# Optimization experiments

Hardware: AMD Instinct MI355X
Metric: run time of the kernel (lower is better)

The kernel has to match this reference:

```python
import jax, jax.numpy as jnp
import numpy as np
import itertools

BINS_NUM = 35
BINS_SIZE = 9
ORDERS = (2, 3, 4, 5)

def _comb_idx(n, k):
    # combinations with replacement of indices 0..n-1, shape [ncomb, k]
    return np.array(list(itertools.combinations_with_replacement(range(n), k)), dtype=np.int32)

_COMB = {k: _comb_idx(BINS_SIZE, k) for k in ORDERS}


def setup_inputs() -> dict:
    key = jax.random.key(0)
    x = jax.random.normal(key, (1024, BINS_NUM * BINS_SIZE), dtype=jnp.float32)
    return {"x": x}


def reference(x) -> jnp.ndarray:
    B = x.shape[0]
    bins = x.reshape(B, BINS_NUM, BINS_SIZE)          # [B, 35, 9]
    parts = [bins]                                     # 'origin' slice first
    for k in ORDERS:
        idx = jnp.asarray(_COMB[k])                    # [ncomb_k, k]
        gathered = bins[:, :, idx]                     # [B, 35, ncomb_k, k]
        parts.append(jnp.prod(gathered, axis=-1))      # [B, 35, ncomb_k]
    # per-bin concat [origin, de2, de3, de4, de5], then flatten bins -> matches
    # torch's outer concat over bins since bin is the leading concat axis here.
    out = jnp.concatenate(parts, axis=-1)              # [B, 35, 2001]
    return out.reshape(B, -1)                          # [B, 70035]
```

## Files before the change

kernel.cpp:

```cpp
#include <hip/hip_runtime.h>

#define BSZ 9
#define NPB 2001
#define N2 45
#define N3 165
#define N4 495
#define O2 9
#define O3 54
#define O4 219
#define ONE_SLOT 714
#define LSZ 720
#define NBLOCKS 2048
#define STRIDE_T (NBLOCKS * 4)

#define WAVE_SYNC() asm volatile("s_waitcnt lgkmcnt(0)" ::: "memory")

constexpr unsigned pslot2(unsigned i, unsigned j) {
    return O2 + i * 9u - i * (i - 1u) / 2u + (j - i);
}

struct Tabs { unsigned short p2[N2]; unsigned short p3[N3]; unsigned short p4[N4]; };
constexpr Tabs make_tabs() {
    Tabs t{};
    { int p = 0;
      for (unsigned i = 0; i < 9; ++i)
          for (unsigned j = i; j < 9; ++j)
              t.p2[p++] = (unsigned short)(i | (j << 8)); }
    { int p = 0;
      for (unsigned a = 0; a < 9; ++a)
          for (unsigned b = a; b < 9; ++b) {
              const unsigned ps = pslot2(a, b);
              for (unsigned c = b; c < 9; ++c)
                  t.p3[p++] = (unsigned short)(ps | (c << 8));
          } }
    { int p = 0; unsigned ts = O3;
      for (unsigned a = 0; a < 9; ++a)
          for (unsigned b = a; b < 9; ++b)
              for (unsigned c = b; c < 9; ++c) {
                  for (unsigned d = c; d < 9; ++d)
                      t.p4[p++] = (unsigned short)(ts | (d << 8));
                  ++ts;
              } }
    return t;
}
__constant__ Tabs g_tabs = make_tabs();

struct Full { unsigned t[NPB]; };
constexpr Full make_full() {
    Full f{};
    for (unsigned j = 0; j < ONE_SLOT; ++j)
        f.t[j] = (4u * j) | ((4u * ONE_SLOT) << 16);
    { int p = ONE_SLOT; unsigned qs = O4;
      for (unsigned a = 0; a < 9; ++a)
          for (unsigned b = a; b < 9; ++b)
              for (unsigned c = b; c < 9; ++c)
                  for (unsigned d = c; d < 9; ++d) {
                      for (unsigned e = d; e < 9; ++e)
                          f.t[p++] = (4u * qs) | ((4u * e) << 16);
                      ++qs;
                  } }
    return f;
}
__constant__ Full g_full = make_full();

__global__ __launch_bounds__(256) void poly_expand_kernel(
        const float* __restrict__ x, float* __restrict__ out, int ntask) {
    __shared__ float L[4][LSZ];
    const int wave = threadIdx.x >> 6;
    const int lane = threadIdx.x & 63;
    const int w0 = blockIdx.x * 4 + wave;
    if (w0 >= ntask) return;
    float* const Lw = L[wave];

    const unsigned o     = (unsigned)w0 & 3u;
    const unsigned a     = (4u - o) & 3u;
    const unsigned mA    = (ONE_SLOT - a) >> 2;
    const unsigned mB0   = (ONE_SLOT - a + 3u) >> 2;
    const unsigned Mfull = (NPB - a) >> 2;
    float* const Ls = Lw + o;
    const char* const Lc = (const char*)Ls;
    const float4* const Af4 = (const float4*)(Lw + o + a);

    const unsigned t2 = (lane < N2) ? (unsigned)g_tabs.p2[lane] : 0u;
    unsigned t3[3], t4[8];
    #pragma unroll
    for (int k = 0; k < 3; ++k) { const int s = lane + 64 * k;
        t3[k] = (s < N3) ? (unsigned)g_tabs.p3[s] : 0u; }
    #pragma unroll
    for (int k = 0; k < 8; ++k) { const int s = lane + 64 * k;
        t4[k] = (s < N4) ? (unsigned)g_tabs.p4[s] : 0u; }

    const unsigned jb0 = a + 4u * mB0;
    unsigned bpk[6][4];
    #pragma unroll
    for (int k = 0; k < 6; ++k) {
        const unsigned idx = (unsigned)lane + 64u * k;
        #pragma unroll
        for (int e = 0; e < 4; ++e)
            bpk[k][e] = (idx < 321u) ? g_full.t[jb0 + 4u * idx + (unsigned)e] : 0u;
    }

    const unsigned z1s = a + 4u * mA, z1n = 4u * (mB0 - mA);
    const unsigned z2s = a + 4u * Mfull, z2n = (unsigned)NPB - z2s;
    int jm = -1;
    if ((unsigned)lane < a)                 jm = lane;
    else if ((unsigned)lane < a + z1n)      jm = (int)(z1s + ((unsigned)lane - a));
    else if ((unsigned)lane < a + z1n + z2n) jm = (int)(z2s + ((unsigned)lane - a - z1n));
    const unsigned mpk = (jm >= 0) ? g_full.t[jm] : 0u;

    for (int task = w0; task < ntask; task += STRIDE_T) {
        const unsigned rb = (unsigned)task * (unsigned)NPB;
        WAVE_SYNC();

        if (lane < 9)       Ls[lane] = x[(size_t)task * BSZ + lane];
        else if (lane == 9) Ls[ONE_SLOT] = 1.0f;
        WAVE_SYNC();
        if (lane < N2) Ls[O2 + lane] = Ls[t2 & 255u] * Ls[t2 >> 8];
        WAVE_SYNC();
        #pragma unroll
        for (int k = 0; k < 3; ++k) { const int s = lane + 64 * k;
            if (s < N3) Ls[O3 + s] = Ls[t3[k] & 255u] * Ls[t3[k] >> 8]; }
        WAVE_SYNC();
        #pragma unroll
        for (int k = 0; k < 8; ++k) { const int s = lane + 64 * k;
            if (s < N4) Ls[O4 + s] = Ls[t4[k] & 255u] * Ls[t4[k] >> 8]; }
        WAVE_SYNC();

        float4* const po4 = (float4*)(out + rb + a);

        #pragma unroll
        for (int k = 0; k < 3; ++k) {
            const unsigned m = (unsigned)lane + 64u * k;
            if (m < mA) po4[m] = Af4[m];
        }
        #pragma unroll
        for (int k = 0; k < 6; ++k) {
            const unsigned idx = (unsigned)lane + 64u * k;
            if (idx < 321u) {
                float r[4];
                #pragma unroll
                for (int e = 0; e < 4; ++e) {
                    const unsigned pk = bpk[k][e];
                    r[e] = *(const float*)(Lc + (pk & 0xFFFFu)) *
                           *(const float*)(Lc + (pk >> 16));
                }
                po4[mB0 + idx] = make_float4(r[0], r[1], r[2], r[3]);
            }
        }
        if (jm >= 0)
            out[rb + (unsigned)jm] = *(const float*)(Lc + (mpk & 0xFFFFu)) *
                                     *(const float*)(Lc + (mpk >> 16));
    }
}

extern "C" void kernel_launch(void* const* d_in, const int* in_sizes, int n_in,
                              void* d_out, int out_size, void* d_ws, size_t ws_size,
                              hipStream_t stream) {
    const float* x = (const float*)d_in[0];
    float* out = (float*)d_out;
    const int ntask = in_sizes[0] / BSZ;
    int blocks = (ntask + 3) / 4;
    if (blocks > NBLOCKS) blocks = NBLOCKS;
    poly_expand_kernel<<<blocks, 256, 0, stream>>>(x, out, ntask);
}
```

Before: 52.03 us.

## Use nontemporal output stores, prefetch next task's inputs, and shrink grid

Output stores, including the float4 vector stores and the scalar tail stores, now use nontemporal builtins so the write-only ~287MB output stream does not pollute caches. The 9 input values for the next task are loaded into a register during the current iteration, which hides global load latency. The constant-one slot is written once outside the loop, and the block count drops from 2048 to 1792. Nontemporal stores may change write-combining behavior, and the smaller grid changes how tasks are spread across CUs.

```diff
diff --git a/kernel.cpp b/kernel.cpp
--- a/kernel.cpp
+++ b/kernel.cpp
@@ -10,10 +10,19 @@
 #define O4 219
 #define ONE_SLOT 714
 #define LSZ 720
-#define NBLOCKS 2048
+#define NBLOCKS 1792
 #define STRIDE_T (NBLOCKS * 4)
 
 #define WAVE_SYNC() asm volatile("s_waitcnt lgkmcnt(0)" ::: "memory")
+
+typedef float vfloat4 __attribute__((ext_vector_type(4)));
+
+__device__ __forceinline__ void st_nt4(float* p, vfloat4 v) {
+    __builtin_nontemporal_store(v, (vfloat4*)p);
+}
+__device__ __forceinline__ void st_nt1(float* p, float v) {
+    __builtin_nontemporal_store(v, p);
+}
 
 constexpr unsigned pslot2(unsigned i, unsigned j) {
     return O2 + i * 9u - i * (i - 1u) / 2u + (j - i);
@@ -79,7 +88,7 @@
     const unsigned Mfull = (NPB - a) >> 2;
     float* const Ls = Lw + o;
     const char* const Lc = (const char*)Ls;
-    const float4* const Af4 = (const float4*)(Lw + o + a);
+    const float* const Afp = Lw + o + a;
 
     const unsigned t2 = (lane < N2) ? (unsigned)g_tabs.p2[lane] : 0u;
     unsigned t3[3], t4[8];
@@ -108,12 +117,20 @@
     else if ((unsigned)lane < a + z1n + z2n) jm = (int)(z2s + ((unsigned)lane - a - z1n));
     const unsigned mpk = (jm >= 0) ? g_full.t[jm] : 0u;
 
+    if (lane == 9) Ls[ONE_SLOT] = 1.0f;
+
+    float xreg = 0.0f;
+    if (lane < 9) xreg = x[(size_t)w0 * BSZ + lane];
+
     for (int task = w0; task < ntask; task += STRIDE_T) {
         const unsigned rb = (unsigned)task * (unsigned)NPB;
         WAVE_SYNC();
 
-        if (lane < 9)       Ls[lane] = x[(size_t)task * BSZ + lane];
-        else if (lane == 9) Ls[ONE_SLOT] = 1.0f;
+        if (lane < 9) Ls[lane] = xreg;
+        {
+            const int nxt = task + STRIDE_T;
+            if (lane < 9 && nxt < ntask) xreg = x[(size_t)nxt * BSZ + lane];
+        }
         WAVE_SYNC();
         if (lane < N2) Ls[O2 + lane] = Ls[t2 & 255u] * Ls[t2 >> 8];
         WAVE_SYNC();
@@ -126,30 +143,34 @@
             if (s < N4) Ls[O4 + s] = Ls[t4[k] & 255u] * Ls[t4[k] >> 8]; }
         WAVE_SYNC();
 
-        float4* const po4 = (float4*)(out + rb + a);
+        float* const po = out + rb + a;
 
         #pragma unroll
         for (int k = 0; k < 3; ++k) {
             const unsigned m = (unsigned)lane + 64u * k;
-            if (m < mA) po4[m] = Af4[m];
+            if (m < mA) {
+                const vfloat4 v = *(const vfloat4*)(Afp + 4u * m);
+                st_nt4(po + 4u * m, v);
+            }
         }
         #pragma unroll
         for (int k = 0; k < 6; ++k) {
             const unsigned idx = (unsigned)lane + 64u * k;
             if (idx < 321u) {
-                float r[4];
+                vfloat4 r;
                 #pragma unroll
                 for (int e = 0; e < 4; ++e) {
                     const unsigned pk = bpk[k][e];
                     r[e] = *(const float*)(Lc + (pk & 0xFFFFu)) *
                            *(const float*)(Lc + (pk >> 16));
                 }
-                po4[mB0 + idx] = make_float4(r[0], r[1], r[2], r[3]);
+                st_nt4(po + 4u * (mB0 + idx), r);
             }
         }
         if (jm >= 0)
-            out[rb + (unsigned)jm] = *(const float*)(Lc + (mpk & 0xFFFFu)) *
-                                     *(const float*)(Lc + (mpk >> 16));
+            st_nt1(out + rb + (unsigned)jm,
+                   *(const float*)(Lc + (mpk & 0xFFFFu)) *
+                   *(const float*)(Lc + (mpk >> 16)));
     }
 }
 
```

Result: slower. 79.38 us (+52.5%).
